# Optimization experiments

Measured on AMD Instinct MI355X. Metric: run time of the kernel, lower is better.

The kernel has to match this reference:

```python
import jax, jax.numpy as jnp
import numpy as np

B, T_IN, T_OUT = 64, 512, 500
N_MEL, ENC_DIM, ATT_DIM = 80, 512, 128
ATT_RNN, DEC_RNN, PRENET = 1024, 1024, 256
N_FILT, KSIZE = 32, 31
PAD = (KSIZE - 1) // 2


def setup_inputs() -> dict:
    key = jax.random.key(0)
    ks = jax.random.split(key, 20)
    g = lambda i, shape, s: jax.random.normal(ks[i], shape, jnp.float32) * s
    return {
        'memory': g(0, (B, T_IN, ENC_DIM), 1.0),
        'decoder_inputs': g(1, (B, N_MEL, T_OUT), 1.0),
        'memory_lengths': jax.random.randint(ks[2], (B,), T_IN // 2, T_IN + 1).astype(jnp.int32),
        'prenet_w1': g(3, (PRENET, N_MEL), 0.05),
        'prenet_w2': g(4, (PRENET, PRENET), 0.05),
        'att_wih': g(5, (4 * ATT_RNN, PRENET + ENC_DIM), 0.02),
        'att_whh': g(6, (4 * ATT_RNN, ATT_RNN), 0.02),
        'att_bih': jnp.zeros((4 * ATT_RNN,), jnp.float32),
        'att_bhh': jnp.zeros((4 * ATT_RNN,), jnp.float32),
        'wq': g(7, (ATT_DIM, ATT_RNN), 0.03),
        'wm': g(8, (ATT_DIM, ENC_DIM), 0.03),
        'v': g(9, (ATT_DIM,), 0.05),
        'loc_conv': g(10, (N_FILT, 2, KSIZE), 0.05),
        'loc_dense': g(11, (ATT_DIM, N_FILT), 0.05),
        'dec_wih': g(12, (4 * DEC_RNN, ATT_RNN + ENC_DIM), 0.02),
        'dec_whh': g(13, (4 * DEC_RNN, DEC_RNN), 0.02),
        'dec_bih': jnp.zeros((4 * DEC_RNN,), jnp.float32),
        'dec_bhh': jnp.zeros((4 * DEC_RNN,), jnp.float32),
        'proj_w': g(14, (N_MEL, DEC_RNN + ENC_DIM), 0.02),
        'proj_b': jnp.zeros((N_MEL,), jnp.float32),
        'gate_w': g(15, (1, DEC_RNN + ENC_DIM), 0.02),
        'gate_b': jnp.zeros((1,), jnp.float32),
    }


def _lstm_cell(x, h, c, wih, whh, bih, bhh):
    gates = x @ wih.T + bih + h @ whh.T + bhh
    i, f, g, o = jnp.split(gates, 4, axis=-1)
    c_new = jax.nn.sigmoid(f) * c + jax.nn.sigmoid(i) * jnp.tanh(g)
    h_new = jax.nn.sigmoid(o) * jnp.tanh(c_new)
    return h_new, c_new


def _forward(memory, decoder_inputs, memory_lengths, prenet_w1, prenet_w2,
             att_wih, att_whh, att_bih, att_bhh, wq, wm, v, loc_conv, loc_dense,
             dec_wih, dec_whh, dec_bih, dec_bhh, proj_w, proj_b, gate_w, gate_b):
    # padding mask: True at padded encoder positions
    mask = jnp.arange(T_IN)[None, :] >= memory_lengths[:, None]  # [B, T_in]
    processed_memory = memory @ wm.T  # [B, T_in, ATT_DIM]

    # parse decoder inputs -> [T_out, B, N_MEL]; prepend all-zero go frame
    di = jnp.transpose(decoder_inputs, (2, 0, 1))
    di = jnp.concatenate([jnp.zeros((1, B, N_MEL), di.dtype), di], axis=0)

    # prenet (dropout p=0.5 is always active in the original; deterministic key)
    dk1, dk2 = jax.random.split(jax.random.key(42))
    x = jax.nn.relu(di @ prenet_w1.T)
    x = x * jax.random.bernoulli(dk1, 0.5, x.shape).astype(x.dtype) * 2.0
    x = jax.nn.relu(x @ prenet_w2.T)
    x = x * jax.random.bernoulli(dk2, 0.5, x.shape).astype(x.dtype) * 2.0  # [T_out+1, B, PRENET]

    def step(carry, x_t):
        ah, ac, dh, dc, aw, awc, ctx = carry
        # attention LSTM
        ah, ac = _lstm_cell(jnp.concatenate([x_t, ctx], -1), ah, ac,
                            att_wih, att_whh, att_bih, att_bhh)
        # location-sensitive attention
        awcat = jnp.stack([aw, awc], axis=1)  # [B, 2, T_in]
        loc = jax.lax.conv_general_dilated(awcat, loc_conv, (1,), [(PAD, PAD)],
                                           dimension_numbers=('NCH', 'OIH', 'NCH'))  # [B, F, T_in]
        loc = jnp.einsum('bft,af->bta', loc, loc_dense)  # [B, T_in, ATT_DIM]
        pq = (ah @ wq.T)[:, None, :]  # [B, 1, ATT_DIM]
        energies = jnp.tanh(pq + loc + processed_memory) @ v  # [B, T_in]
        energies = jnp.where(mask, -jnp.inf, energies)
        aw = jax.nn.softmax(energies, axis=1)
        ctx = jnp.einsum('bt,btd->bd', aw, memory)
        awc = awc + aw
        # decoder LSTM
        dh, dc = _lstm_cell(jnp.concatenate([ah, ctx], -1), dh, dc,
                            dec_wih, dec_whh, dec_bih, dec_bhh)
        dhc = jnp.concatenate([dh, ctx], -1)  # [B, DEC_RNN+ENC_DIM]
        mel = dhc @ proj_w.T + proj_b  # [B, N_MEL]
        gate = (dhc @ gate_w.T + gate_b)[:, 0]  # [B]
        return (ah, ac, dh, dc, aw, awc, ctx), (mel, gate, aw)

    z = lambda *s: jnp.zeros(s, jnp.float32)
    init = (z(B, ATT_RNN), z(B, ATT_RNN), z(B, DEC_RNN), z(B, DEC_RNN),
            z(B, T_IN), z(B, T_IN), z(B, ENC_DIM))
    _, (mels, gates, aws) = jax.lax.scan(step, init, x[:T_OUT])
    mel_outputs = jnp.transpose(mels, (1, 0, 2)).reshape(B, -1, N_MEL)  # [B, T_out, N_MEL]
    gate_outputs = gates.T  # [B, T_out]
    alignments = jnp.transpose(aws, (1, 0, 2))  # [B, T_out, T_in]
    return mel_outputs, gate_outputs, alignments


def reference(memory, decoder_inputs, memory_lengths, prenet_w1, prenet_w2,
              att_wih, att_whh, att_bih, att_bhh, wq, wm, v, loc_conv, loc_dense,
              dec_wih, dec_whh, dec_bih, dec_bhh, proj_w, proj_b, gate_w, gate_b):
    return _forward(memory, decoder_inputs, memory_lengths, prenet_w1, prenet_w2,
                    att_wih, att_whh, att_bih, att_bhh, wq, wm, v, loc_conv, loc_dense,
                    dec_wih, dec_whh, dec_bih, dec_bhh, proj_w, proj_b, gate_w, gate_b)
```

## Files before the change

kernel.cpp:

```cpp
#include <hip/hip_runtime.h>
#include <cstdint>
#include <cstddef>

#define NB    64
#define TIN   512
#define TOUT  500
#define NMEL  80
#define ENC   512
#define ATTD  128
#define ARNN  1024
#define DRNN  1024
#define PREN  256
#define NFILT 32
#define KSZ   31
#define CPAD  15

#define MEL_OFF  0
#define GATE_OFF 2560000
#define ALGN_OFF 2592000

#define X_SZ      8192000
#define PM_SZ     4194304
#define G1_SZ     1048576
#define G2_SZ     1048576
#define XATT_SZ   98304
#define XDEC_SZ   163840
#define AC_SZ     65536
#define DC_SZ     65536
#define AW_SZ     32768
#define AWC_SZ    32768
#define TAILH_SZ  49152
#define TAILL_SZ  49152
#define XDH_SZ    81920
#define XDL_SZ    81920
#define PQ_SZ     8192
#define EN_SZ     32768
#define MASK_N    8208384

#define K1TOT   1792
#define K2TOT   2560
#define NCH1    56
#define NCH2    80
#define PK1_N   14680064
#define PK2_N   20971520

typedef unsigned short u16;
typedef __attribute__((ext_vector_type(8))) short bf16x8;
typedef __attribute__((ext_vector_type(4))) float f32x4;

__device__ __forceinline__ uint32_t rotl32(uint32_t v, int r) { return (v << r) | (v >> (32 - r)); }

__device__ __forceinline__ float sigf(float x) { return 1.f / (1.f + __expf(-x)); }
__device__ __forceinline__ float tanhf_fast(float x) {
    float ax = fabsf(x);
    float t = 1.f - 2.f / (__expf(2.f * ax) + 1.f);
    return copysignf(t, x);
}

__device__ __forceinline__ void split1(float v, u16& h, u16& l) {
    uint32_t u = __float_as_uint(v);
    h = (u16)(u >> 16);
    float r = v - __uint_as_float(u & 0xFFFF0000u);
    uint32_t ru = __float_as_uint(r);
    ru += 0x7FFFu + ((ru >> 16) & 1u);
    l = (u16)(ru >> 16);
}

__device__ __forceinline__ void split8(float4 f0, float4 f1, bf16x8& h, bf16x8& l) {
    float v[8] = { f0.x, f0.y, f0.z, f0.w, f1.x, f1.y, f1.z, f1.w };
#pragma unroll
    for (int i = 0; i < 8; ++i) {
        uint32_t u = __float_as_uint(v[i]);
        h[i] = (short)(u >> 16);
        float r = v[i] - __uint_as_float(u & 0xFFFF0000u);
        uint32_t ru = __float_as_uint(r);
        ru += 0x7FFFu + ((ru >> 16) & 1u);
        l[i] = (short)(ru >> 16);
    }
}

#define MFMA16(a, b, c) __builtin_amdgcn_mfma_f32_16x16x32_bf16(a, b, c, 0, 0, 0)

__device__ void tf_block(uint32_t k1, uint32_t k2, uint32_t& x0, uint32_t& x1) {
    uint32_t ks0 = k1, ks1 = k2, ks2 = k1 ^ k2 ^ 0x1BD11BDAu;
    x0 += ks0; x1 += ks1;
#define TFR(r) { x0 += x1; x1 = rotl32(x1, r); x1 ^= x0; }
    TFR(13) TFR(15) TFR(26) TFR(6)   x0 += ks1; x1 += ks2 + 1u;
    TFR(17) TFR(29) TFR(16) TFR(24)  x0 += ks2; x1 += ks0 + 2u;
    TFR(13) TFR(15) TFR(26) TFR(6)   x0 += ks0; x1 += ks1 + 3u;
    TFR(17) TFR(29) TFR(16) TFR(24)  x0 += ks1; x1 += ks2 + 4u;
    TFR(13) TFR(15) TFR(26) TFR(6)   x0 += ks2; x1 += ks0 + 5u;
#undef TFR
}

__global__ __launch_bounds__(256) void mask_kernel(unsigned char* m1, unsigned char* m2) {
    int i = blockIdx.x * 256 + threadIdx.x;
    if (i >= MASK_N) return;
    uint32_t a0 = 0u, a1 = 0u; tf_block(0u, 42u, a0, a1);
    uint32_t b0 = 0u, b1 = 1u; tf_block(0u, 42u, b0, b1);
    uint32_t x0, x1;
    x0 = 0u; x1 = (uint32_t)i; tf_block(a0, a1, x0, x1);
    m1[i] = ((x0 ^ x1) >> 31) == 0u;
    x0 = 0u; x1 = (uint32_t)i; tf_block(b0, b1, x0, x1);
    m2[i] = ((x0 ^ x1) >> 31) == 0u;
}

__global__ __launch_bounds__(256) void prenet1_kernel(
    const float* __restrict__ dec_in, const float* __restrict__ w1,
    const unsigned char* __restrict__ m1, float* __restrict__ x)
{
    int r = blockIdx.x;
    int t = r >> 6, b = r & 63;
    int tid = threadIdx.x;
    __shared__ float ds[NMEL];
    if (tid < NMEL) ds[tid] = (t == 0) ? 0.f : dec_in[(size_t)b * 40000 + tid * 500 + (t - 1)];
    __syncthreads();
    float acc = 0.f;
    const float* w = w1 + tid * NMEL;
#pragma unroll
    for (int k = 0; k < NMEL; ++k) acc += ds[k] * w[k];
    acc = fmaxf(acc, 0.f);
    int flat = r * 256 + tid;
    x[flat] = m1[flat] ? acc * 2.f : 0.f;
}

__global__ __launch_bounds__(256) void prenet2_kernel(
    const float* __restrict__ w2, const unsigned char* __restrict__ m2, float* x)
{
    int r = blockIdx.x;
    int tid = threadIdx.x;
    __shared__ float xs[PREN];
    xs[tid] = x[r * 256 + tid];
    __syncthreads();
    float acc = 0.f;
    const float* w = w2 + tid * PREN;
#pragma unroll 8
    for (int k = 0; k < PREN; ++k) acc += xs[k] * w[k];
    acc = fmaxf(acc, 0.f);
    int flat = r * 256 + tid;
    x[flat] = m2[flat] ? acc * 2.f : 0.f;
}

__global__ __launch_bounds__(128) void pm_kernel(
    const float* __restrict__ memory, const float* __restrict__ wm, float* __restrict__ pm)
{
    int b = blockIdx.x, t = blockIdx.y;
    int tid = threadIdx.x;
    __shared__ float ms[ENC];
    for (int i = tid; i < ENC; i += 128) ms[i] = memory[(size_t)b * (TIN * ENC) + (size_t)t * ENC + i];
    __syncthreads();
    float acc = 0.f;
    const float* w = wm + tid * ENC;
#pragma unroll 8
    for (int k = 0; k < ENC; ++k) acc += ms[k] * w[k];
    pm[(size_t)b * (TIN * ATTD) + t * ATTD + tid] = acc;
}

__global__ __launch_bounds__(256) void wpack_kernel(
    const float* __restrict__ w1, int K1, const float* __restrict__ w2, int K2,
    u16* __restrict__ dst)
{
    const int K = K1 + K2;
    int idx = blockIdx.x * 256 + threadIdx.x;
    if (idx >= 4096 * K) return;
    int n = idx / K, k = idx % K;
    float v = (k < K1) ? w1[n * K1 + k] : w2[n * K2 + (k - K1)];
    u16 h, l;
    split1(v, h, l);
    int tile = n >> 4, kc = k >> 5;
    int lane = (n & 15) + (((k & 31) >> 3) << 4);
    size_t off = ((size_t)(tile * (K >> 5) + kc) * 2) * 512 + lane * 8 + (k & 7);
    dst[off] = h;
    dst[off + 512] = l;
}

struct SmemGemm { float Xs[32][68]; float Ws[32][68]; };

__device__ void gemm_phase(
    const float* __restrict__ X1, int ldx1, int kx1,
    const float* __restrict__ X2, int ldx2,
    const float* __restrict__ W1, int ldw1, int kw1,
    const float* __restrict__ W2, int ldw2,
    float* __restrict__ outp, int Kq, int blk, SmemGemm& s)
{
    const int tid = threadIdx.x;
    const int n0 = (blk & 63) * 64;
    const int ks = blk >> 6;
    const int kbeg = ks * Kq;
    const int tn = tid & 15, tm = tid >> 4;
    float acc[4][4];
#pragma unroll
    for (int i = 0; i < 4; ++i)
#pragma unroll
        for (int j = 0; j < 4; ++j) acc[i][j] = 0.f;

#pragma unroll 1
    for (int k0 = kbeg; k0 < kbeg + Kq; k0 += 32) {
#pragma unroll
        for (int i = 0; i < 8; ++i) {
            int flat = i * 256 + tid;
            int m = flat >> 5, c = flat & 31;
            int k = k0 + c;
            s.Xs[c][m] = (k < kx1) ? X1[m * ldx1 + k] : X2[m * ldx2 + (k - kx1)];
        }
#pragma unroll
        for (int i = 0; i < 8; ++i) {
            int flat = i * 256 + tid;
            int r = flat >> 5, c = flat & 31;
            int k = k0 + c;
            int n = n0 + r;
            s.Ws[c][r] = (k < kw1) ? W1[n * ldw1 + k] : W2[n * ldw2 + (k - kw1)];
        }
        __syncthreads();
#pragma unroll
        for (int kk = 0; kk < 32; ++kk) {
            float4 xv = *(const float4*)&s.Xs[kk][tm * 4];
            float4 wv = *(const float4*)&s.Ws[kk][tn * 4];
            float xr[4] = { xv.x, xv.y, xv.z, xv.w };
            float wr[4] = { wv.x, wv.y, wv.z, wv.w };
#pragma unroll
            for (int i = 0; i < 4; ++i)
#pragma unroll
                for (int j = 0; j < 4; ++j) acc[i][j] += xr[i] * wr[j];
        }
        __syncthreads();
    }
    float* o = outp + (size_t)ks * 64 * 4096;
#pragma unroll
    for (int i = 0; i < 4; ++i)
#pragma unroll
        for (int j = 0; j < 4; ++j)
            o[(tm * 4 + i) * 4096 + (n0 + tn * 4 + j)] = acc[i][j];
}

__global__ __launch_bounds__(256, 2) void pair_gemm(
    const float* __restrict__ xcat_dec,
    const float* __restrict__ dec_wih, const float* __restrict__ dec_whh,
    float* __restrict__ g2,
    const float* __restrict__ x, const float* __restrict__ xcat_att,
    const float* __restrict__ att_wih, const float* __restrict__ att_whh,
    float* __restrict__ g1, int t)
{
    __shared__ __align__(16) SmemGemm sm;
    const int blk = blockIdx.x;
    if (blk < 256) {
        if (t < 0) return;
        gemm_phase(xcat_dec, 2560, 2560, xcat_dec, 2560,
                   dec_wih, 1536, 1536, dec_whh, 1024, g2, 640, blk, sm);
    } else {
        const int tn = t + 1;
        if (tn >= TOUT) return;
        gemm_phase(x + (size_t)tn * (NB * PREN), PREN, PREN, xcat_att, 1536,
                   att_wih, 768, 768, att_whh, 1024, g1, 448, blk - 256, sm);
    }
}

__device__ __forceinline__ void mfma_tile_run(
    const u16* __restrict__ Ah, const u16* __restrict__ Al, int aoff,
    const float* __restrict__ xr,
    const u16* __restrict__ bp, int kc_beg, int nchunk, int kc_wrap_at, int kc_wrap_to,
    f32x4& acc, int lane)
{
    const int kg = lane >> 4;
#pragma unroll 4
    for (int i = 0; i < nchunk; ++i) {
        int kc = kc_beg + i;
        if (kc >= kc_wrap_at) kc = kc_wrap_to + (kc - kc_wrap_at);
        const int k = kc * 32 + kg * 8;
        bf16x8 ah, al;
        if (xr && k < 256) {
            float4 f0 = *(const float4*)(xr + k);
            float4 f1 = *(const float4*)(xr + k + 4);
            split8(f0, f1, ah, al);
        } else {
            ah = *(const bf16x8*)(Ah + (k - aoff));
            al = *(const bf16x8*)(Al + (k - aoff));
        }
        const u16* c0 = bp + (size_t)kc * 1024;
        bf16x8 bh = *(const bf16x8*)c0;
        bf16x8 bl = *(const bf16x8*)(c0 + 512);
        acc = MFMA16(ah, bh, acc); acc = MFMA16(ah, bl, acc); acc = MFMA16(al, bh, acc);
    }
}

__device__ __forceinline__ void mfma_store(float* o, f32x4 acc, int tile, int wave, int lane)
{
    const int n0 = tile * 16;
    const int mbase = wave * 16 + (lane >> 4) * 4;
    const int lr = lane & 15;
#pragma unroll
    for (int r = 0; r < 4; ++r)
        o[(mbase + r) * 4096 + n0 + lr] = acc[r];
}

__device__ void energies_body(
    int b, int tc,
    const float* __restrict__ aw, const float* __restrict__ awc,
    const float* __restrict__ lc, const float* __restrict__ ld,
    const float* __restrict__ vvec, const float* __restrict__ pq,
    const float* __restrict__ pm, float* __restrict__ energ)
{
    const int t0 = tc * 64;
    const int tid = threadIdx.x;
    __shared__ float awin[96], awcin[96];
    __shared__ float lcs[NFILT * 62];
    __shared__ float locs[64 * 33];
    __shared__ float pqs[ATTD], vs[ATTD];
    __shared__ float ldm[ATTD * 33];

    for (int i = tid; i < 94; i += 256) {
        int t = t0 + i - CPAD;
        bool ok = (t >= 0 && t < TIN);
        awin[i]  = ok ? aw[b * TIN + t]  : 0.f;
        awcin[i] = ok ? awc[b * TIN + t] : 0.f;
    }
    for (int i = tid; i < NFILT * 62; i += 256) lcs[i] = lc[i];
    for (int i = tid; i < ATTD * NFILT; i += 256) ldm[(i >> 5) * 33 + (i & 31)] = ld[i];
    if (tid < ATTD) { pqs[tid] = pq[b * ATTD + tid]; vs[tid] = vvec[tid]; }
    __syncthreads();

    for (int idx = tid; idx < 64 * 32; idx += 256) {
        int tl = idx >> 5, f = idx & 31;
        const float* w0 = lcs + f * 62;
        float s = 0.f;
#pragma unroll
        for (int k = 0; k < KSZ; ++k)
            s += awin[tl + k] * w0[k] + awcin[tl + k] * w0[31 + k];
        locs[tl * 33 + f] = s;
    }
    __syncthreads();

    const int tl = tid >> 2, q = tid & 3;
    const int a0 = q * 32;
    const float* pmrow = pm + (size_t)b * (TIN * ATTD) + (size_t)(t0 + tl) * ATTD + a0;
    const float* lt = locs + tl * 33;
    float4 pv[8];
#pragma unroll
    for (int u = 0; u < 8; ++u) pv[u] = *(const float4*)&pmrow[u * 4];
    float e = 0.f;
#pragma unroll
    for (int aa = 0; aa < 32; ++aa) {
        int a = a0 + aa;
        float sv = pqs[a] + ((const float*)pv)[aa];
        const float* lrow = ldm + a * 33;
#pragma unroll
        for (int f = 0; f < NFILT; ++f) sv += lt[f] * lrow[f];
        e += vs[a] * tanhf_fast(sv);
    }
    e += __shfl_xor(e, 1);
    e += __shfl_xor(e, 2);
    if (q == 0) energ[b * TIN + t0 + tl] = e;
}

__global__ __launch_bounds__(256) void fused_mid(
    const float* __restrict__ aw, const float* __restrict__ awc,
    const float* __restrict__ lc, const float* __restrict__ ld,
    const float* __restrict__ vvec, const float* __restrict__ pq,
    const float* __restrict__ pm, float* __restrict__ energ,
    const u16* __restrict__ xdech, const u16* __restrict__ xdecl,
    const u16* __restrict__ pk2, float* __restrict__ g2,
    const float* __restrict__ x,
    const u16* __restrict__ tailh, const u16* __restrict__ taill,
    const u16* __restrict__ pk1, float* __restrict__ g1, int t)
{
    const int blk = blockIdx.x;
    if (blk < 512) {
        if (t < 0) return;
        energies_body(blk >> 3, blk & 7, aw, awc, lc, ld, vvec, pq, pm, energ);
        return;
    }
    const int tid = threadIdx.x;
    const int wave = tid >> 6, lane = tid & 63;
    const int mrow = wave * 16 + (lane & 15);
    f32x4 acc = {0.f, 0.f, 0.f, 0.f};

    if (blk < 1024) {
        if (t < 0) return;
        const int r = blk - 512;
        const int tile = r & 255, ks = r >> 8;
        const u16* bp = pk2 + (size_t)tile * NCH2 * 1024 + lane * 8;
        mfma_tile_run(xdech + mrow * 2560, xdecl + mrow * 2560, 0, nullptr,
                      bp, ks == 0 ? 0 : 48, 32, 1000, 0, acc, lane);
        mfma_store(g2 + (size_t)ks * 262144, acc, tile, wave, lane);
    } else {
        const int tn = t + 1;
        if (tn >= TOUT) return;
        const int r = blk - 1024;
        const int tile = r & 255, ks = r >> 8;
        const u16* bp = pk1 + (size_t)tile * NCH1 * 1024 + lane * 8;
        const float* xr = x + ((size_t)tn * 64 + mrow) * 256;
        mfma_tile_run(tailh + mrow * 1536, taill + mrow * 1536, 256, xr,
                      bp, ks == 0 ? 24 : 44, 20, 56, 0, acc, lane);
        mfma_store(g1 + (size_t)ks * 262144, acc, tile, wave, lane);
    }
}

__global__ __launch_bounds__(256) void gemm_late(
    const u16* __restrict__ xdech, const u16* __restrict__ xdecl,
    const u16* __restrict__ pk2, float* __restrict__ g2,
    const u16* __restrict__ tailh, const u16* __restrict__ taill,
    const u16* __restrict__ pk1, float* __restrict__ g1, int t)
{
    const int blk = blockIdx.x;
    const int tid = threadIdx.x;
    const int wave = tid >> 6, lane = tid & 63;
    const int mrow = wave * 16 + (lane & 15);
    f32x4 acc = {0.f, 0.f, 0.f, 0.f};

    if (blk < 256) {
        if (t < 0) return;
        const int tile = blk;
        const u16* bp = pk2 + (size_t)tile * NCH2 * 1024 + lane * 8;
        mfma_tile_run(xdech + mrow * 2560, xdecl + mrow * 2560, 0, nullptr,
                      bp, 32, 16, 1000, 0, acc, lane);
        mfma_store(g2 + (size_t)2 * 262144, acc, tile, wave, lane);
    } else {
        const int tn = t + 1;
        if (tn >= TOUT) return;
        const int tile = blk - 256;
        const u16* bp = pk1 + (size_t)tile * NCH1 * 1024 + lane * 8;
        mfma_tile_run(tailh + mrow * 1536, taill + mrow * 1536, 256, nullptr,
                      bp, 8, 16, 1000, 0, acc, lane);
        mfma_store(g1 + (size_t)2 * 262144, acc, tile, wave, lane);
    }
}

__global__ __launch_bounds__(256) void pair_pw(
    const float* __restrict__ g1, const float* __restrict__ att_bih, const float* __restrict__ att_bhh,
    float* __restrict__ ac, float* __restrict__ xcat_att, float* __restrict__ xcat_dec,
    const float* __restrict__ wq, float* __restrict__ pq,
    const float* __restrict__ g2, const float* __restrict__ dec_bih, const float* __restrict__ dec_bhh,
    float* __restrict__ dc, const float* __restrict__ proj_w, const float* __restrict__ proj_b,
    const float* __restrict__ gate_w, const float* __restrict__ gate_b,
    float* __restrict__ out,
    u16* __restrict__ tailh, u16* __restrict__ taill,
    u16* __restrict__ xdech, u16* __restrict__ xdecl,
    int nsplit, int t)
{
    const int tid = threadIdx.x;
    __shared__ float sbuf[1536];
    __shared__ float red[256];

    if (blockIdx.x < 64) {
        if (t >= TOUT) return;
        const int b = blockIdx.x;
#pragma unroll
        for (int q = 0; q < 4; ++q) {
            int j = q * 256 + tid;
            float gi = att_bih[j] + att_bhh[j];
            float gf = att_bih[1024 + j] + att_bhh[1024 + j];
            float gg = att_bih[2048 + j] + att_bhh[2048 + j];
            float go = att_bih[3072 + j] + att_bhh[3072 + j];
            for (int s = 0; s < nsplit; ++s) {
                const float* g = g1 + (size_t)s * 262144 + b * 4096;
                gi += g[j]; gf += g[1024 + j]; gg += g[2048 + j]; go += g[3072 + j];
            }
            float c = sigf(gf) * ac[b * 1024 + j] + sigf(gi) * tanhf_fast(gg);
            float h = sigf(go) * tanhf_fast(c);
            ac[b * 1024 + j] = c;
            xcat_att[b * 1536 + 512 + j] = h;
            xcat_dec[b * 2560 + j] = h;
            u16 hh, hl; split1(h, hh, hl);
            tailh[b * 1536 + 512 + j] = hh;  taill[b * 1536 + 512 + j] = hl;
            xdech[b * 2560 + j] = hh;        xdecl[b * 2560 + j] = hl;
            sbuf[j] = h;
        }
        __syncthreads();
        const int a = tid & 127, half = tid >> 7;
        const float* wr = wq + a * 1024 + half * 512;
        const float* hh = sbuf + half * 512;
        float s0 = 0.f, s1 = 0.f, s2 = 0.f, s3 = 0.f;
#pragma unroll 4
        for (int k = 0; k < 512; k += 16) {
            float4 w0 = *(const float4*)&wr[k],      h0 = *(const float4*)&hh[k];
            float4 w1 = *(const float4*)&wr[k + 4],  h1 = *(const float4*)&hh[k + 4];
            float4 w2 = *(const float4*)&wr[k + 8],  h2 = *(const float4*)&hh[k + 8];
            float4 w3 = *(const float4*)&wr[k + 12], h3 = *(const float4*)&hh[k + 12];
            s0 += h0.x * w0.x + h0.y * w0.y + h0.z * w0.z + h0.w * w0.w;
            s1 += h1.x * w1.x + h1.y * w1.y + h1.z * w1.z + h1.w * w1.w;
            s2 += h2.x * w2.x + h2.y * w2.y + h2.z * w2.z + h2.w * w2.w;
            s3 += h3.x * w3.x + h3.y * w3.y + h3.z * w3.z + h3.w * w3.w;
        }
        red[tid] = (s0 + s1) + (s2 + s3);
        __syncthreads();
        if (half == 0) pq[b * 128 + a] = red[a] + red[a + 128];
    } else {
        if (t < 1) return;
        const int b = blockIdx.x - 64;
        const int ts = t - 1;
#pragma unroll
        for (int q = 0; q < 4; ++q) {
            int j = q * 256 + tid;
            float gi = dec_bih[j] + dec_bhh[j];
            float gf = dec_bih[1024 + j] + dec_bhh[1024 + j];
            float gg = dec_bih[2048 + j] + dec_bhh[2048 + j];
            float go = dec_bih[3072 + j] + dec_bhh[3072 + j];
            for (int s = 0; s < nsplit; ++s) {
                const float* g = g2 + (size_t)s * 262144 + b * 4096;
                gi += g[j]; gf += g[1024 + j]; gg += g[2048 + j]; go += g[3072 + j];
            }
            float c = sigf(gf) * dc[b * 1024 + j] + sigf(gi) * tanhf_fast(gg);
            float h = sigf(go) * tanhf_fast(c);
            dc[b * 1024 + j] = c;
            xcat_dec[b * 2560 + 1536 + j] = h;
            u16 hh, hl; split1(h, hh, hl);
            xdech[b * 2560 + 1536 + j] = hh;  xdecl[b * 2560 + 1536 + j] = hl;
            sbuf[j] = h;
        }
        for (int i = tid; i < 512; i += 256) sbuf[1024 + i] = xcat_dec[b * 2560 + 1024 + i];
        __syncthreads();
        const int o = tid >> 1, half = tid & 1;
        float accv = 0.f;
        if (o <= 80) {
            const float* w = (o < 80) ? (proj_w + o * 1536) : gate_w;
            const float* sv = sbuf + half * 768;
            const float* wv = w + half * 768;
            float s0 = 0.f, s1 = 0.f, s2 = 0.f, s3 = 0.f;
#pragma unroll 4
            for (int k = 0; k < 768; k += 16) {
                float4 a0 = *(const float4*)&sv[k],      b0 = *(const float4*)&wv[k];
                float4 a1 = *(const float4*)&sv[k + 4],  b1 = *(const float4*)&wv[k + 4];
                float4 a2 = *(const float4*)&sv[k + 8],  b2 = *(const float4*)&wv[k + 8];
                float4 a3 = *(const float4*)&sv[k + 12], b3 = *(const float4*)&wv[k + 12];
                s0 += a0.x * b0.x + a0.y * b0.y + a0.z * b0.z + a0.w * b0.w;
                s1 += a1.x * b1.x + a1.y * b1.y + a1.z * b1.z + a1.w * b1.w;
                s2 += a2.x * b2.x + a2.y * b2.y + a2.z * b2.z + a2.w * b2.w;
                s3 += a3.x * b3.x + a3.y * b3.y + a3.z * b3.z + a3.w * b3.w;
            }
            accv = (s0 + s1) + (s2 + s3);
        }
        red[tid] = accv;
        __syncthreads();
        if (half == 0 && o <= 80) {
            float r = red[tid] + red[tid + 1];
            if (o < 80)
                out[MEL_OFF + (size_t)b * (TOUT * NMEL) + (size_t)ts * NMEL + o] = r + proj_b[o];
            else
                out[GATE_OFF + (size_t)b * TOUT + ts] = r + gate_b[0];
        }
    }
}

__global__ __launch_bounds__(256) void energies_kernel(
    const float* __restrict__ aw, const float* __restrict__ awc,
    const float* __restrict__ lc, const float* __restrict__ ld,
    const float* __restrict__ vvec, const float* __restrict__ pq,
    const float* __restrict__ pm, float* __restrict__ energ)
{
    energies_body(blockIdx.x >> 3, blockIdx.x & 7, aw, awc, lc, ld, vvec, pq, pm, energ);
}

__global__ __launch_bounds__(256) void softmax_ctx_kernel(
    const float* __restrict__ energ, const int* __restrict__ mlen,
    const float* __restrict__ memory,
    float* __restrict__ aw, float* __restrict__ awc,
    float* __restrict__ out_align, int t_step,
    float* __restrict__ xcat_att, float* __restrict__ xcat_dec,
    u16* __restrict__ tailh, u16* __restrict__ taill,
    u16* __restrict__ xdech, u16* __restrict__ xdecl)
{
    const int b = blockIdx.x >> 3, dq = blockIdx.x & 7;
    const int tid = threadIdx.x;
    const int len = mlen[b];
    __shared__ float es[TIN];
    __shared__ float red[256];

    float e1 = (tid < len) ? energ[b * TIN + tid] : -INFINITY;
    float e2 = (tid + 256 < len) ? energ[b * TIN + tid + 256] : -INFINITY;
    red[tid] = fmaxf(e1, e2);
    __syncthreads();
    for (int s = 128; s > 0; s >>= 1) {
        if (tid < s) red[tid] = fmaxf(red[tid], red[tid + s]);
        __syncthreads();
    }
    const float mx = red[0];
    __syncthreads();
    float p1 = __expf(e1 - mx);
    float p2 = __expf(e2 - mx);
    red[tid] = p1 + p2;
    __syncthreads();
    for (int s = 128; s > 0; s >>= 1) {
        if (tid < s) red[tid] += red[tid + s];
        __syncthreads();
    }
    const float inv = 1.f / red[0];
    p1 *= inv; p2 *= inv;
    es[tid] = p1; es[tid + 256] = p2;
    __syncthreads();

    if (tid < 64) {
        int tt = dq * 64 + tid;
        float p = es[tt];
        aw[b * TIN + tt] = p;
        awc[b * TIN + tt] += p;
        out_align[(size_t)b * (TOUT * TIN) + (size_t)t_step * TIN + tt] = p;
    }

    const int d = dq * 64 + (tid & 63), th = tid >> 6;
    const float* mb = memory + (size_t)b * (TIN * ENC);
    float accv = 0.f;
#pragma unroll 4
    for (int tt = th * 128; tt < th * 128 + 128; ++tt)
        accv += es[tt] * mb[(size_t)tt * ENC + d];
    red[tid] = accv;
    __syncthreads();
    if (tid < 64) {
        float cv = (red[tid] + red[tid + 64]) + (red[tid + 128] + red[tid + 192]);
        int dd = dq * 64 + tid;
        xcat_att[b * 1536 + dd] = cv;
        xcat_dec[b * 2560 + 1024 + dd] = cv;
        u16 h, l; split1(cv, h, l);
        tailh[b * 1536 + dd] = h;        taill[b * 1536 + dd] = l;
        xdech[b * 2560 + 1024 + dd] = h; xdecl[b * 2560 + 1024 + dd] = l;
    }
}

extern "C" void kernel_launch(void* const* d_in, const int* in_sizes, int n_in,
                              void* d_out, int out_size, void* d_ws, size_t ws_size,
                              hipStream_t stream) {
    const float* memory   = (const float*)d_in[0];
    const float* dec_in   = (const float*)d_in[1];
    const int*   mlen     = (const int*)d_in[2];
    const float* pw1      = (const float*)d_in[3];
    const float* pw2      = (const float*)d_in[4];
    const float* att_wih  = (const float*)d_in[5];
    const float* att_whh  = (const float*)d_in[6];
    const float* att_bih  = (const float*)d_in[7];
    const float* att_bhh  = (const float*)d_in[8];
    const float* wq       = (const float*)d_in[9];
    const float* wm       = (const float*)d_in[10];
    const float* v        = (const float*)d_in[11];
    const float* loc_conv = (const float*)d_in[12];
    const float* loc_dense= (const float*)d_in[13];
    const float* dec_wih  = (const float*)d_in[14];
    const float* dec_whh  = (const float*)d_in[15];
    const float* dec_bih  = (const float*)d_in[16];
    const float* dec_bhh  = (const float*)d_in[17];
    const float* proj_w   = (const float*)d_in[18];
    const float* proj_b   = (const float*)d_in[19];
    const float* gate_w   = (const float*)d_in[20];
    const float* gate_b   = (const float*)d_in[21];
    float* out = (float*)d_out;

    float* x        = (float*)d_ws;
    float* pm       = x + X_SZ;
    float* g1       = pm + PM_SZ;
    float* g2       = g1 + G1_SZ;
    float* xcat_att = g2 + G2_SZ;
    float* xcat_dec = xcat_att + XATT_SZ;
    float* ac       = xcat_dec + XDEC_SZ;
    float* dc       = ac + AC_SZ;
    float* aw       = dc + DC_SZ;
    float* awc      = aw + AW_SZ;
    float* tailh_f  = awc + AWC_SZ;
    float* taill_f  = tailh_f + TAILH_SZ;
    float* xdech_f  = taill_f + TAILL_SZ;
    float* xdecl_f  = xdech_f + XDH_SZ;
    float* pq       = xdecl_f + XDL_SZ;
    float* energ    = pq + PQ_SZ;
    unsigned char* m1 = (unsigned char*)(energ + EN_SZ);
    unsigned char* m2 = m1 + MASK_N;
    u16* pk1 = (u16*)(m2 + MASK_N);
    u16* pk2 = pk1 + PK1_N;

    u16* tailh = (u16*)tailh_f;  u16* taill = (u16*)taill_f;
    u16* xdech = (u16*)xdech_f;  u16* xdecl = (u16*)xdecl_f;

    size_t need_base = (size_t)(m2 + MASK_N - (unsigned char*)d_ws);
    size_t need_full = (size_t)((unsigned char*)(pk2 + PK2_N) - (unsigned char*)d_ws);
    if (ws_size < need_base) return;
    const bool use_mfma = (ws_size >= need_full);
    const int nsplit = use_mfma ? 3 : 4;

    size_t state_floats = (size_t)XATT_SZ + XDEC_SZ + AC_SZ + DC_SZ + AW_SZ + AWC_SZ
                        + TAILH_SZ + TAILL_SZ + XDH_SZ + XDL_SZ;
    hipMemsetAsync(xcat_att, 0, state_floats * sizeof(float), stream);

    mask_kernel<<<(MASK_N + 255) / 256, 256, 0, stream>>>(m1, m2);
    prenet1_kernel<<<TOUT * NB, 256, 0, stream>>>(dec_in, pw1, m1, x);
    prenet2_kernel<<<TOUT * NB, 256, 0, stream>>>(pw2, m2, x);
    pm_kernel<<<dim3(NB, TIN), 128, 0, stream>>>(memory, wm, pm);
    if (use_mfma) {
        wpack_kernel<<<(4096 * K1TOT + 255) / 256, 256, 0, stream>>>(att_wih, 768, att_whh, 1024, pk1);
        wpack_kernel<<<(4096 * K2TOT + 255) / 256, 256, 0, stream>>>(dec_wih, 1536, dec_whh, 1024, pk2);
    }

    float* out_align = out + ALGN_OFF;

    if (use_mfma) {
        fused_mid<<<1536, 256, 0, stream>>>(aw, awc, loc_conv, loc_dense, v, pq, pm, energ,
                                            xdech, xdecl, pk2, g2, x, tailh, taill, pk1, g1, -1);
        gemm_late<<<512, 256, 0, stream>>>(xdech, xdecl, pk2, g2, tailh, taill, pk1, g1, -1);
    } else {
        pair_gemm<<<512, 256, 0, stream>>>(xcat_dec, dec_wih, dec_whh, g2,
                                           x, xcat_att, att_wih, att_whh, g1, -1);
    }

    for (int t = 0; t < TOUT; ++t) {
        pair_pw<<<128, 256, 0, stream>>>(g1, att_bih, att_bhh, ac, xcat_att, xcat_dec, wq, pq,
                                         g2, dec_bih, dec_bhh, dc, proj_w, proj_b,
                                         gate_w, gate_b, out, tailh, taill, xdech, xdecl,
                                         nsplit, t);
        if (use_mfma) {
            fused_mid<<<1536, 256, 0, stream>>>(aw, awc, loc_conv, loc_dense, v, pq, pm, energ,
                                                xdech, xdecl, pk2, g2, x, tailh, taill, pk1, g1, t);
            softmax_ctx_kernel<<<512, 256, 0, stream>>>(energ, mlen, memory, aw, awc, out_align, t,
                                                        xcat_att, xcat_dec, tailh, taill, xdech, xdecl);
            gemm_late<<<512, 256, 0, stream>>>(xdech, xdecl, pk2, g2, tailh, taill, pk1, g1, t);
        } else {
            energies_kernel<<<512, 256, 0, stream>>>(aw, awc, loc_conv, loc_dense, v, pq, pm, energ);
            softmax_ctx_kernel<<<512, 256, 0, stream>>>(energ, mlen, memory, aw, awc, out_align, t,
                                                        xcat_att, xcat_dec, tailh, taill, xdech, xdecl);
            pair_gemm<<<512, 256, 0, stream>>>(xcat_dec, dec_wih, dec_whh, g2,
                                               x, xcat_att, att_wih, att_whh, g1, t);
        }
    }
    pair_pw<<<128, 256, 0, stream>>>(g1, att_bih, att_bhh, ac, xcat_att, xcat_dec, wq, pq,
                                     g2, dec_bih, dec_bhh, dc, proj_w, proj_b,
                                     gate_w, gate_b, out, tailh, taill, xdech, xdecl,
                                     nsplit, TOUT);
}
```

Before: 53.88 ms.

## Fuse attention energies, softmax and context into a per-batch block of mid kernel

Replaces the fused_mid plus softmax_ctx_kernel pair with a single mega_mid kernel. The first 64 blocks each handle one batch row end to end: location conv, energies, masked softmax, alignment writes and the context reduction over memory. The remaining blocks run the same MFMA gate GEMM tiles as before. This removes one kernel launch and the round-trip of the energy buffer through global memory on every decoder step. In exchange, attention work now runs on only 64 blocks with long serial loops, and it runs alongside GEMM blocks that read neighbouring parts of the same state buffers.

```diff
diff --git a/kernel.cpp b/kernel.cpp
--- a/kernel.cpp
+++ b/kernel.cpp
@@ -352,47 +352,169 @@
     if (q == 0) energ[b * TIN + t0 + tl] = e;
 }
 
-__global__ __launch_bounds__(256) void fused_mid(
-    const float* __restrict__ aw, const float* __restrict__ awc,
+struct MegaP1 {
+    float awin[544]; float awcin[544];
+    float lcs[NFILT * 62];
+    float ldm[ATTD * 33];
+    float locs[64 * 33];
+    float pqs[ATTD]; float vs[ATTD];
+};
+struct MegaP2 { float ms[8][ENC]; };
+union MegaU { MegaP1 p1; MegaP2 p2; };
+
+__global__ __launch_bounds__(256) void mega_mid(
+    const float* __restrict__ aw, float* __restrict__ awc,
     const float* __restrict__ lc, const float* __restrict__ ld,
     const float* __restrict__ vvec, const float* __restrict__ pq,
-    const float* __restrict__ pm, float* __restrict__ energ,
-    const u16* __restrict__ xdech, const u16* __restrict__ xdecl,
+    const float* __restrict__ pm, const int* __restrict__ mlen,
+    const float* __restrict__ memory, float* __restrict__ out_align,
+    float* __restrict__ aw_out,
+    float* __restrict__ xcat_att, float* __restrict__ xcat_dec,
+    u16* __restrict__ tailh, u16* __restrict__ taill,
+    u16* __restrict__ xdech, u16* __restrict__ xdecl,
     const u16* __restrict__ pk2, float* __restrict__ g2,
     const float* __restrict__ x,
-    const u16* __restrict__ tailh, const u16* __restrict__ taill,
     const u16* __restrict__ pk1, float* __restrict__ g1, int t)
 {
     const int blk = blockIdx.x;
-    if (blk < 512) {
-        if (t < 0) return;
-        energies_body(blk >> 3, blk & 7, aw, awc, lc, ld, vvec, pq, pm, energ);
+    const int tid = threadIdx.x;
+
+    if (blk >= 64) {
+        const int wave = tid >> 6, lane = tid & 63;
+        const int mrow = wave * 16 + (lane & 15);
+        f32x4 acc = {0.f, 0.f, 0.f, 0.f};
+        if (blk < 576) {
+            if (t < 0) return;
+            const int r = blk - 64;
+            const int tile = r & 255, ks = r >> 8;
+            const u16* bp = pk2 + (size_t)tile * NCH2 * 1024 + lane * 8;
+            mfma_tile_run(xdech + mrow * 2560, xdecl + mrow * 2560, 0, nullptr,
+                          bp, ks == 0 ? 0 : 48, 32, 1000, 0, acc, lane);
+            mfma_store(g2 + (size_t)ks * 262144, acc, tile, wave, lane);
+        } else {
+            const int tn = t + 1;
+            if (tn >= TOUT) return;
+            const int r = blk - 576;
+            const int tile = r & 255, ks = r >> 8;
+            const u16* bp = pk1 + (size_t)tile * NCH1 * 1024 + lane * 8;
+            const float* xr = x + ((size_t)tn * 64 + mrow) * 256;
+            mfma_tile_run(tailh + mrow * 1536, taill + mrow * 1536, 256, xr,
+                          bp, ks == 0 ? 24 : 44, 20, 56, 0, acc, lane);
+            mfma_store(g1 + (size_t)ks * 262144, acc, tile, wave, lane);
+        }
         return;
     }
-    const int tid = threadIdx.x;
-    const int wave = tid >> 6, lane = tid & 63;
-    const int mrow = wave * 16 + (lane & 15);
-    f32x4 acc = {0.f, 0.f, 0.f, 0.f};
-
-    if (blk < 1024) {
-        if (t < 0) return;
-        const int r = blk - 512;
-        const int tile = r & 255, ks = r >> 8;
-        const u16* bp = pk2 + (size_t)tile * NCH2 * 1024 + lane * 8;
-        mfma_tile_run(xdech + mrow * 2560, xdecl + mrow * 2560, 0, nullptr,
-                      bp, ks == 0 ? 0 : 48, 32, 1000, 0, acc, lane);
-        mfma_store(g2 + (size_t)ks * 262144, acc, tile, wave, lane);
-    } else {
-        const int tn = t + 1;
-        if (tn >= TOUT) return;
-        const int r = blk - 1024;
-        const int tile = r & 255, ks = r >> 8;
-        const u16* bp = pk1 + (size_t)tile * NCH1 * 1024 + lane * 8;
-        const float* xr = x + ((size_t)tn * 64 + mrow) * 256;
-        mfma_tile_run(tailh + mrow * 1536, taill + mrow * 1536, 256, xr,
-                      bp, ks == 0 ? 24 : 44, 20, 56, 0, acc, lane);
-        mfma_store(g1 + (size_t)ks * 262144, acc, tile, wave, lane);
-    }
+
+    if (t < 0) return;
+    const int b = blk;
+    __shared__ __align__(16) MegaU mu;
+    __shared__ float es[TIN];
+    __shared__ float red[256];
+
+    for (int i = tid; i < 542; i += 256) {
+        int tt = i - CPAD;
+        bool ok = (tt >= 0 && tt < TIN);
+        mu.p1.awin[i]  = ok ? aw[b * TIN + tt]  : 0.f;
+        mu.p1.awcin[i] = ok ? awc[b * TIN + tt] : 0.f;
+    }
+    for (int i = tid; i < NFILT * 62; i += 256) mu.p1.lcs[i] = lc[i];
+    for (int i = tid; i < ATTD * NFILT; i += 256) mu.p1.ldm[(i >> 5) * 33 + (i & 31)] = ld[i];
+    if (tid < ATTD) { mu.p1.pqs[tid] = pq[b * ATTD + tid]; mu.p1.vs[tid] = vvec[tid]; }
+    __syncthreads();
+
+#pragma unroll 1
+    for (int tc = 0; tc < 8; ++tc) {
+        const int t0 = tc * 64;
+        for (int idx = tid; idx < 64 * 32; idx += 256) {
+            int tl = idx >> 5, f = idx & 31;
+            const float* w0 = mu.p1.lcs + f * 62;
+            float s = 0.f;
+#pragma unroll
+            for (int k = 0; k < KSZ; ++k)
+                s += mu.p1.awin[t0 + tl + k] * w0[k] + mu.p1.awcin[t0 + tl + k] * w0[31 + k];
+            mu.p1.locs[tl * 33 + f] = s;
+        }
+        __syncthreads();
+        const int tl = tid >> 2, q = tid & 3;
+        const int a0 = q * 32;
+        const float* pmrow = pm + (size_t)b * (TIN * ATTD) + (size_t)(t0 + tl) * ATTD + a0;
+        const float* lt = mu.p1.locs + tl * 33;
+        float4 pv[8];
+#pragma unroll
+        for (int u = 0; u < 8; ++u) pv[u] = *(const float4*)&pmrow[u * 4];
+        float e = 0.f;
+#pragma unroll
+        for (int aa = 0; aa < 32; ++aa) {
+            int a = a0 + aa;
+            float sv = mu.p1.pqs[a] + ((const float*)pv)[aa];
+            const float* lrow = mu.p1.ldm + a * 33;
+#pragma unroll
+            for (int f = 0; f < NFILT; ++f) sv += lt[f] * lrow[f];
+            e += mu.p1.vs[a] * tanhf_fast(sv);
+        }
+        e += __shfl_xor(e, 1);
+        e += __shfl_xor(e, 2);
+        if (q == 0) es[t0 + tl] = e;
+        __syncthreads();
+    }
+
+    const int len = mlen[b];
+    float e1 = (tid < len) ? es[tid] : -INFINITY;
+    float e2 = (tid + 256 < len) ? es[tid + 256] : -INFINITY;
+    red[tid] = fmaxf(e1, e2);
+    __syncthreads();
+    for (int s = 128; s > 0; s >>= 1) {
+        if (tid < s) red[tid] = fmaxf(red[tid], red[tid + s]);
+        __syncthreads();
+    }
+    const float mx = red[0];
+    __syncthreads();
+    float p1 = __expf(e1 - mx);
+    float p2 = __expf(e2 - mx);
+    red[tid] = p1 + p2;
+    __syncthreads();
+    for (int s = 128; s > 0; s >>= 1) {
+        if (tid < s) red[tid] += red[tid + s];
+        __syncthreads();
+    }
+    const float inv = 1.f / red[0];
+    p1 *= inv; p2 *= inv;
+    es[tid] = p1; es[tid + 256] = p2;
+
+    aw_out[b * TIN + tid] = p1;        aw_out[b * TIN + tid + 256] = p2;
+    awc[b * TIN + tid] += p1;          awc[b * TIN + tid + 256] += p2;
+    size_t ao = (size_t)b * (TOUT * TIN) + (size_t)t * TIN;
+    out_align[ao + tid] = p1;          out_align[ao + tid + 256] = p2;
+
+    float c1 = 0.f, c2 = 0.f;
+    const float* mb = memory + (size_t)b * (TIN * ENC);
+#pragma unroll 1
+    for (int tc = 0; tc < TIN; tc += 8) {
+        __syncthreads();
+#pragma unroll
+        for (int i = 0; i < 16; ++i) {
+            int flat = i * 256 + tid;
+            int tt = flat >> 9, d = flat & 511;
+            mu.p2.ms[tt][d] = mb[(size_t)(tc + tt) * ENC + d];
+        }
+        __syncthreads();
+#pragma unroll
+        for (int j = 0; j < 8; ++j) {
+            float a_ = es[tc + j];
+            c1 += a_ * mu.p2.ms[j][tid];
+            c2 += a_ * mu.p2.ms[j][tid + 256];
+        }
+    }
+    xcat_att[b * 1536 + tid] = c1;
+    xcat_att[b * 1536 + 256 + tid] = c2;
+    xcat_dec[b * 2560 + 1024 + tid] = c1;
+    xcat_dec[b * 2560 + 1024 + 256 + tid] = c2;
+    u16 h1, l1, h2, l2;
+    split1(c1, h1, l1); split1(c2, h2, l2);
+    tailh[b * 1536 + tid] = h1;        taill[b * 1536 + tid] = l1;
+    tailh[b * 1536 + 256 + tid] = h2;  taill[b * 1536 + 256 + tid] = l2;
+    xdech[b * 2560 + 1024 + tid] = h1;        xdecl[b * 2560 + 1024 + tid] = l1;
+    xdech[b * 2560 + 1024 + 256 + tid] = h2;  xdecl[b * 2560 + 1024 + 256 + tid] = l2;
 }
 
 __global__ __launch_bounds__(256) void gemm_late(
@@ -688,8 +810,10 @@
     float* out_align = out + ALGN_OFF;
 
     if (use_mfma) {
-        fused_mid<<<1536, 256, 0, stream>>>(aw, awc, loc_conv, loc_dense, v, pq, pm, energ,
-                                            xdech, xdecl, pk2, g2, x, tailh, taill, pk1, g1, -1);
+        mega_mid<<<1088, 256, 0, stream>>>(aw, awc, loc_conv, loc_dense, v, pq, pm, mlen,
+                                           memory, out_align, aw,
+                                           xcat_att, xcat_dec, tailh, taill, xdech, xdecl,
+                                           pk2, g2, x, pk1, g1, -1);
         gemm_late<<<512, 256, 0, stream>>>(xdech, xdecl, pk2, g2, tailh, taill, pk1, g1, -1);
     } else {
         pair_gemm<<<512, 256, 0, stream>>>(xcat_dec, dec_wih, dec_whh, g2,
@@ -702,10 +826,10 @@
                                          gate_w, gate_b, out, tailh, taill, xdech, xdecl,
                                          nsplit, t);
         if (use_mfma) {
-            fused_mid<<<1536, 256, 0, stream>>>(aw, awc, loc_conv, loc_dense, v, pq, pm, energ,
-                                                xdech, xdecl, pk2, g2, x, tailh, taill, pk1, g1, t);
-            softmax_ctx_kernel<<<512, 256, 0, stream>>>(energ, mlen, memory, aw, awc, out_align, t,
-                                                        xcat_att, xcat_dec, tailh, taill, xdech, xdecl);
+            mega_mid<<<1088, 256, 0, stream>>>(aw, awc, loc_conv, loc_dense, v, pq, pm, mlen,
+                                               memory, out_align, aw,
+                                               xcat_att, xcat_dec, tailh, taill, xdech, xdecl,
+                                               pk2, g2, x, pk1, g1, t);
             gemm_late<<<512, 256, 0, stream>>>(xdech, xdecl, pk2, g2, tailh, taill, pk1, g1, t);
         } else {
             energies_kernel<<<512, 256, 0, stream>>>(aw, awc, loc_conv, loc_dense, v, pq, pm, energ);
```

Result: slower. 148.1 ms (+174.9%).

## Move attention-LSTM input GEMM blocks from energies kernel into softmax-context kernel

Applied to the files above, without the earlier changes.

Splits the attention-RNN partial GEMM (pk1 blocks) out of the fused energies/decoder-GEMM launch and co-schedules it with the softmax/context kernel in a new fused_sm launch. This rebalances work across the per-step launches, shrinking fused_mid to 1024 blocks and filling softmax_ctx's launch with independent MFMA work. Because the pk1 GEMM reads tailh/taill, which are written during softmax (the context part), there is a possible read-before-write hazard within the same launch.

```diff
diff --git a/kernel.cpp b/kernel.cpp
--- a/kernel.cpp
+++ b/kernel.cpp
@@ -358,14 +358,11 @@
     const float* __restrict__ vvec, const float* __restrict__ pq,
     const float* __restrict__ pm, float* __restrict__ energ,
     const u16* __restrict__ xdech, const u16* __restrict__ xdecl,
-    const u16* __restrict__ pk2, float* __restrict__ g2,
-    const float* __restrict__ x,
-    const u16* __restrict__ tailh, const u16* __restrict__ taill,
-    const u16* __restrict__ pk1, float* __restrict__ g1, int t)
+    const u16* __restrict__ pk2, float* __restrict__ g2, int t)
 {
     const int blk = blockIdx.x;
+    if (t < 0) return;
     if (blk < 512) {
-        if (t < 0) return;
         energies_body(blk >> 3, blk & 7, aw, awc, lc, ld, vvec, pq, pm, energ);
         return;
     }
@@ -373,25 +370,97 @@
     const int wave = tid >> 6, lane = tid & 63;
     const int mrow = wave * 16 + (lane & 15);
     f32x4 acc = {0.f, 0.f, 0.f, 0.f};
-
-    if (blk < 1024) {
-        if (t < 0) return;
-        const int r = blk - 512;
-        const int tile = r & 255, ks = r >> 8;
-        const u16* bp = pk2 + (size_t)tile * NCH2 * 1024 + lane * 8;
-        mfma_tile_run(xdech + mrow * 2560, xdecl + mrow * 2560, 0, nullptr,
-                      bp, ks == 0 ? 0 : 48, 32, 1000, 0, acc, lane);
-        mfma_store(g2 + (size_t)ks * 262144, acc, tile, wave, lane);
-    } else {
+    const int r = blk - 512;
+    const int tile = r & 255, ks = r >> 8;
+    const u16* bp = pk2 + (size_t)tile * NCH2 * 1024 + lane * 8;
+    mfma_tile_run(xdech + mrow * 2560, xdecl + mrow * 2560, 0, nullptr,
+                  bp, ks == 0 ? 0 : 48, 32, 1000, 0, acc, lane);
+    mfma_store(g2 + (size_t)ks * 262144, acc, tile, wave, lane);
+}
+
+__global__ __launch_bounds__(256) void fused_sm(
+    const float* __restrict__ energ, const int* __restrict__ mlen,
+    const float* __restrict__ memory,
+    float* __restrict__ aw, float* __restrict__ awc,
+    float* __restrict__ out_align, int t,
+    float* __restrict__ xcat_att, float* __restrict__ xcat_dec,
+    u16* __restrict__ tailh, u16* __restrict__ taill,
+    u16* __restrict__ xdech, u16* __restrict__ xdecl,
+    const float* __restrict__ x,
+    const u16* __restrict__ pk1, float* __restrict__ g1)
+{
+    const int blk = blockIdx.x;
+    const int tid = threadIdx.x;
+
+    if (blk >= 512) {
         const int tn = t + 1;
         if (tn >= TOUT) return;
-        const int r = blk - 1024;
+        const int wave = tid >> 6, lane = tid & 63;
+        const int mrow = wave * 16 + (lane & 15);
+        f32x4 acc = {0.f, 0.f, 0.f, 0.f};
+        const int r = blk - 512;
         const int tile = r & 255, ks = r >> 8;
         const u16* bp = pk1 + (size_t)tile * NCH1 * 1024 + lane * 8;
         const float* xr = x + ((size_t)tn * 64 + mrow) * 256;
         mfma_tile_run(tailh + mrow * 1536, taill + mrow * 1536, 256, xr,
                       bp, ks == 0 ? 24 : 44, 20, 56, 0, acc, lane);
         mfma_store(g1 + (size_t)ks * 262144, acc, tile, wave, lane);
+        return;
+    }
+
+    if (t < 0) return;
+    const int b = blk >> 3, dq = blk & 7;
+    const int len = mlen[b];
+    __shared__ float es[TIN];
+    __shared__ float red[256];
+
+    float e1 = (tid < len) ? energ[b * TIN + tid] : -INFINITY;
+    float e2 = (tid + 256 < len) ? energ[b * TIN + tid + 256] : -INFINITY;
+    red[tid] = fmaxf(e1, e2);
+    __syncthreads();
+    for (int s = 128; s > 0; s >>= 1) {
+        if (tid < s) red[tid] = fmaxf(red[tid], red[tid + s]);
+        __syncthreads();
+    }
+    const float mx = red[0];
+    __syncthreads();
+    float p1 = __expf(e1 - mx);
+    float p2 = __expf(e2 - mx);
+    red[tid] = p1 + p2;
+    __syncthreads();
+    for (int s = 128; s > 0; s >>= 1) {
+        if (tid < s) red[tid] += red[tid + s];
+        __syncthreads();
+    }
+    const float inv = 1.f / red[0];
+    p1 *= inv; p2 *= inv;
+    es[tid] = p1; es[tid + 256] = p2;
+    __syncthreads();
+
+    if (tid < 64) {
+        int tt = dq * 64 + tid;
+        float p = es[tt];
+        aw[b * TIN + tt] = p;
+        awc[b * TIN + tt] += p;
+        out_align[(size_t)b * (TOUT * TIN) + (size_t)t * TIN + tt] = p;
+    }
+
+    const int d = dq * 64 + (tid & 63), th = tid >> 6;
+    const float* mb = memory + (size_t)b * (TIN * ENC);
+    float accv = 0.f;
+#pragma unroll 4
+    for (int tt = th * 128; tt < th * 128 + 128; ++tt)
+        accv += es[tt] * mb[(size_t)tt * ENC + d];
+    red[tid] = accv;
+    __syncthreads();
+    if (tid < 64) {
+        float cv = (red[tid] + red[tid + 64]) + (red[tid + 128] + red[tid + 192]);
+        int dd = dq * 64 + tid;
+        xcat_att[b * 1536 + dd] = cv;
+        xcat_dec[b * 2560 + 1024 + dd] = cv;
+        u16 h, l; split1(cv, h, l);
+        tailh[b * 1536 + dd] = h;        taill[b * 1536 + dd] = l;
+        xdech[b * 2560 + 1024 + dd] = h; xdecl[b * 2560 + 1024 + dd] = l;
     }
 }
 
@@ -688,8 +757,9 @@
     float* out_align = out + ALGN_OFF;
 
     if (use_mfma) {
-        fused_mid<<<1536, 256, 0, stream>>>(aw, awc, loc_conv, loc_dense, v, pq, pm, energ,
-                                            xdech, xdecl, pk2, g2, x, tailh, taill, pk1, g1, -1);
+        fused_sm<<<1024, 256, 0, stream>>>(energ, mlen, memory, aw, awc, out_align, -1,
+                                           xcat_att, xcat_dec, tailh, taill, xdech, xdecl,
+                                           x, pk1, g1);
         gemm_late<<<512, 256, 0, stream>>>(xdech, xdecl, pk2, g2, tailh, taill, pk1, g1, -1);
     } else {
         pair_gemm<<<512, 256, 0, stream>>>(xcat_dec, dec_wih, dec_whh, g2,
@@ -702,10 +772,11 @@
                                          gate_w, gate_b, out, tailh, taill, xdech, xdecl,
                                          nsplit, t);
         if (use_mfma) {
-            fused_mid<<<1536, 256, 0, stream>>>(aw, awc, loc_conv, loc_dense, v, pq, pm, energ,
-                                                xdech, xdecl, pk2, g2, x, tailh, taill, pk1, g1, t);
-            softmax_ctx_kernel<<<512, 256, 0, stream>>>(energ, mlen, memory, aw, awc, out_align, t,
-                                                        xcat_att, xcat_dec, tailh, taill, xdech, xdecl);
+            fused_mid<<<1024, 256, 0, stream>>>(aw, awc, loc_conv, loc_dense, v, pq, pm, energ,
+                                                xdech, xdecl, pk2, g2, t);
+            fused_sm<<<1024, 256, 0, stream>>>(energ, mlen, memory, aw, awc, out_align, t,
+                                               xcat_att, xcat_dec, tailh, taill, xdech, xdecl,
+                                               x, pk1, g1);
             gemm_late<<<512, 256, 0, stream>>>(xdech, xdecl, pk2, g2, tailh, taill, pk1, g1, t);
         } else {
             energies_kernel<<<512, 256, 0, stream>>>(aw, awc, loc_conv, loc_dense, v, pq, pm, energ);
```

Measured after the change: 50.24 ms (median of 2 runs). 6.8% less time.
